# Kernel optimization log

Hardware: AMD Instinct MI355X
Metric: run time of the kernel (lower is better)

Reference implementation:

```python
import jax, jax.numpy as jnp
import numpy as np

# Izhikevich params (regular spiking), Euler step with dt=1
A, B_P, C, D, V_TH, DT = 0.02, 0.2, -65.0, 8.0, 30.0, 1.0


def _izh_scan(currents):
    """Run an Izhikevich cell over time. currents: [T, B, F] -> spikes [T, B, F]."""
    shp = currents.shape[1:]
    v0 = jnp.full(shp, C, dtype=currents.dtype)
    u0 = jnp.full(shp, B_P * C, dtype=currents.dtype)

    def step(state, i_t):
        v, u = state
        v = v + DT * (0.04 * v * v + 5.0 * v + 140.0 - u + i_t)
        u = u + DT * A * (B_P * v - u)
        z = (v >= V_TH).astype(currents.dtype)  # spike (heaviside)
        v = jnp.where(z > 0, C, v)               # reset
        u = u + z * D
        return (v, u), z

    (vT, uT), spikes = jax.lax.scan(step, (v0, u0), currents)
    return spikes, (vT, uT)


def setup_inputs() -> dict:
    key = jax.random.key(0)
    k1, k2, k3, k4, k5 = jax.random.split(key, 5)
    T, B, F_IN, F_HID = 2048, 8192, 4, 2
    xs = jax.random.normal(k1, (T, B, F_IN), dtype=jnp.float32)
    # PyTorch Linear default init: U(-1/sqrt(fan_in), 1/sqrt(fan_in)); scaled normal is fine for a baseline
    W_in = jax.random.normal(k2, (F_HID, F_IN), dtype=jnp.float32) * 0.5
    b_in = jax.random.normal(k3, (F_HID,), dtype=jnp.float32) * 0.5
    W_out = jax.random.normal(k4, (1, F_HID), dtype=jnp.float32) * 0.5
    b_out = jax.random.normal(k5, (1,), dtype=jnp.float32) * 0.5
    return {"xs": xs, "W_in": W_in, "b_in": b_in, "W_out": W_out, "b_out": b_out}


def reference(xs, W_in, b_in, W_out, b_out):
    # input linear: [T,B,4] @ [4,2] -> [T,B,2]
    h = jnp.einsum('tbi,oi->tbo', xs, W_in) + b_in
    input_spikes, _ = _izh_scan(h)
    # output linear: [T,B,2] -> [T,B,1]
    y = jnp.einsum('tbi,oi->tbo', input_spikes, W_out) + b_out
    output_spikes, _ = _izh_scan(y)
    return output_spikes
```

## Files before the change

kernel.cpp:

```cpp
#include <hip/hip_runtime.h>

namespace {

constexpr int T   = 2048;
constexpr int B   = 8192;
constexpr int C   = 32;
constexpr int NCH = T / C;
constexpr int RD  = 16;

__device__ __forceinline__ void barrier_nodrain() {
    asm volatile("s_waitcnt lgkmcnt(0)\n\ts_barrier" ::: "memory");
}

struct IzhState {
    float vnp;
    float up;
    bool  spp;
};

__device__ __forceinline__ bool izh_step(IzhState& s, float I) {
#pragma clang fp contract(off)
    const float K0 = ((0.04f * (-65.0f)) * (-65.0f) + (5.0f * (-65.0f))) + 140.0f;
    float m2a = 0.04f * s.vnp;
    float m2  = m2a * s.vnp;
    float f5  = 5.0f * s.vnp;
    float s2A = (m2 + f5) + 140.0f;
    float s3A = s2A - s.up;
    float s4A = s3A + I;
    float vnA = s.vnp + s4A;
    float s3S = K0 - s.up;
    float s4S = s3S + I;
    float vnS = (-65.0f) + s4S;
    float vn  = s.spp ? vnS : vnA;
    bool  sp  = (vn >= 30.0f);
    float m4  = 0.2f * vn;
    float s5  = m4 - s.up;
    float tt  = 0.02f * s5;
    float un  = s.up + tt;
    float d8  = sp ? 8.0f : 0.0f;
    s.up  = un + d8;
    s.vnp = vn;
    s.spp = sp;
    return sp;
}

__global__ __launch_bounds__(192, 1) void izh3b(
    const float* __restrict__ xs,
    const float* __restrict__ W_in, const float* __restrict__ b_in,
    const float* __restrict__ W_out, const float* __restrict__ b_out,
    float* __restrict__ out)
{
    __shared__ float zbuf[2][2][C][64];
    const int lane = threadIdx.x & 63;
    const int wid  = threadIdx.x >> 6;
    const int b    = blockIdx.x * 64 + lane;

    if (wid < 2) {
#pragma clang fp contract(off)
        const float wa = W_in[wid * 4 + 0], wb = W_in[wid * 4 + 1];
        const float wc = W_in[wid * 4 + 2], wd = W_in[wid * 4 + 3];
        const float bi = b_in[wid];
        const float4* xp = reinterpret_cast<const float4*>(xs) + b;

        float4 ring[RD];
#pragma unroll
        for (int i = 0; i < RD; ++i) ring[i] = xp[(size_t)i * B];

        IzhState st{-65.0f, -13.0f, true};
        for (int r = 0; r < NCH; ++r) {
            const int p = r & 1;
#pragma unroll
            for (int j = 0; j < C; ++j) {
                const int t = r * C + j;
                const float4 x = ring[j & (RD - 1)];
                ring[j & (RD - 1)] = xp[(size_t)((t + RD) & (T - 1)) * B];
                float h = (((x.x * wa) + (x.y * wb)) + (x.z * wc)) + (x.w * wd);
                h = h + bi;
                bool sp = izh_step(st, h);
                zbuf[wid][p][j][lane] = sp ? 1.0f : 0.0f;
            }
            barrier_nodrain();
        }
    } else {
#pragma clang fp contract(off)
        const float wo0 = W_out[0], wo1 = W_out[1], bo = b_out[0];
        const float c00 = ((0.0f * wo0) + (0.0f * wo1)) + bo;
        const float c10 = ((1.0f * wo0) + (0.0f * wo1)) + bo;
        const float c01 = ((0.0f * wo0) + (1.0f * wo1)) + bo;
        const float c11 = ((1.0f * wo0) + (1.0f * wo1)) + bo;
        float* op = out + b;
        IzhState st{-65.0f, -13.0f, true};

        auto consume = [&](int kk) {
#pragma clang fp contract(off)
            const int p = kk & 1;
            float z0[C], z1[C];
#pragma unroll
            for (int j = 0; j < C; ++j) {
                z0[j] = zbuf[0][p][j][lane];
                z1[j] = zbuf[1][p][j][lane];
            }
#pragma unroll
            for (int j = 0; j < C; ++j) {
                float yt = (z1[j] != 0.0f) ? c11 : c10;
                float yf = (z1[j] != 0.0f) ? c01 : c00;
                float y  = (z0[j] != 0.0f) ? yt : yf;
                bool spo = izh_step(st, y);
                op[(size_t)(kk * C + j) * B] = spo ? 1.0f : 0.0f;
            }
        };

        for (int r = 0; r < NCH; ++r) {
            if (r > 0) consume(r - 1);
            barrier_nodrain();
        }
        consume(NCH - 1);
    }
}

}

extern "C" void kernel_launch(void* const* d_in, const int* in_sizes, int n_in,
                              void* d_out, int out_size, void* d_ws, size_t ws_size,
                              hipStream_t stream) {
    const float* xs    = (const float*)d_in[0];
    const float* W_in  = (const float*)d_in[1];
    const float* b_in  = (const float*)d_in[2];
    const float* W_out = (const float*)d_in[3];
    const float* b_out = (const float*)d_in[4];
    float* out = (float*)d_out;

    dim3 grid(B / 64), block(192);
    hipLaunchKernelGGL(izh3b, grid, block, 0, stream,
                       xs, W_in, b_in, W_out, b_out, out);
}
```

Baseline: 428.0 us.

## Merge two hidden-neuron waves into one wave using packed float2 math

The two producer wavefronts that each simulated one hidden Izhikevich neuron become a single wavefront that steps both neurons together with two-wide vector float math, which can map to packed FP32 instructions. The block shrinks from three waves to two, and the shared spike buffer is stored as interleaved float2. The xs prefetch ring depth is doubled. The aim is to cut per-step instruction count and halve the redundant global loads of xs, at the cost of more registers and a serial dependency chain per wave that may leave the producer as the bottleneck.

```diff
diff --git a/kernel.cpp b/kernel.cpp
--- a/kernel.cpp
+++ b/kernel.cpp
@@ -6,10 +6,51 @@
 constexpr int B   = 8192;
 constexpr int C   = 32;
 constexpr int NCH = T / C;
-constexpr int RD  = 16;
+constexpr int RD  = 32;
+
+typedef float v2f __attribute__((ext_vector_type(2)));
 
 __device__ __forceinline__ void barrier_nodrain() {
     asm volatile("s_waitcnt lgkmcnt(0)\n\ts_barrier" ::: "memory");
+}
+
+struct IzhState2 {
+    v2f  vnp;
+    v2f  up;
+    bool sx;
+    bool sy;
+};
+
+__device__ __forceinline__ v2f izh_step2(IzhState2& s, v2f I) {
+#pragma clang fp contract(off)
+    const float K0 = ((0.04f * (-65.0f)) * (-65.0f) + (5.0f * (-65.0f))) + 140.0f;
+    v2f m2a = 0.04f * s.vnp;
+    v2f m2  = m2a * s.vnp;
+    v2f f5  = 5.0f * s.vnp;
+    v2f s2A = (m2 + f5) + 140.0f;
+    v2f s3A = s2A - s.up;
+    v2f s4A = s3A + I;
+    v2f vnA = s.vnp + s4A;
+    v2f s3S = K0 - s.up;
+    v2f s4S = s3S + I;
+    v2f vnS = (-65.0f) + s4S;
+    v2f vn;
+    vn.x = s.sx ? vnS.x : vnA.x;
+    vn.y = s.sy ? vnS.y : vnA.y;
+    bool nx = vn.x >= 30.0f;
+    bool ny = vn.y >= 30.0f;
+    v2f m4 = 0.2f * vn;
+    v2f s5 = m4 - s.up;
+    v2f tt = 0.02f * s5;
+    v2f un = s.up + tt;
+    v2f d8;
+    d8.x = nx ? 8.0f : 0.0f;
+    d8.y = ny ? 8.0f : 0.0f;
+    s.up  = un + d8;
+    s.vnp = vn;
+    s.sx  = nx;
+    s.sy  = ny;
+    return d8 * 0.125f;
 }
 
 struct IzhState {
@@ -44,29 +85,35 @@
     return sp;
 }
 
-__global__ __launch_bounds__(192, 1) void izh3b(
+__global__ __launch_bounds__(128, 1) void izh2w(
     const float* __restrict__ xs,
     const float* __restrict__ W_in, const float* __restrict__ b_in,
     const float* __restrict__ W_out, const float* __restrict__ b_out,
     float* __restrict__ out)
 {
-    __shared__ float zbuf[2][2][C][64];
+    __shared__ v2f zbuf[2][C][64];
     const int lane = threadIdx.x & 63;
     const int wid  = threadIdx.x >> 6;
     const int b    = blockIdx.x * 64 + lane;
 
-    if (wid < 2) {
+    if (wid == 0) {
 #pragma clang fp contract(off)
-        const float wa = W_in[wid * 4 + 0], wb = W_in[wid * 4 + 1];
-        const float wc = W_in[wid * 4 + 2], wd = W_in[wid * 4 + 3];
-        const float bi = b_in[wid];
+        const v2f wa = { W_in[0], W_in[4] };
+        const v2f wb = { W_in[1], W_in[5] };
+        const v2f wc = { W_in[2], W_in[6] };
+        const v2f wd = { W_in[3], W_in[7] };
+        const v2f bi = { b_in[0], b_in[1] };
         const float4* xp = reinterpret_cast<const float4*>(xs) + b;
 
         float4 ring[RD];
 #pragma unroll
         for (int i = 0; i < RD; ++i) ring[i] = xp[(size_t)i * B];
 
-        IzhState st{-65.0f, -13.0f, true};
+        IzhState2 st;
+        st.vnp = (v2f){-65.0f, -65.0f};
+        st.up  = (v2f){-13.0f, -13.0f};
+        st.sx = true; st.sy = true;
+
         for (int r = 0; r < NCH; ++r) {
             const int p = r & 1;
 #pragma unroll
@@ -74,10 +121,9 @@
                 const int t = r * C + j;
                 const float4 x = ring[j & (RD - 1)];
                 ring[j & (RD - 1)] = xp[(size_t)((t + RD) & (T - 1)) * B];
-                float h = (((x.x * wa) + (x.y * wb)) + (x.z * wc)) + (x.w * wd);
+                v2f h = (((x.x * wa) + (x.y * wb)) + (x.z * wc)) + (x.w * wd);
                 h = h + bi;
-                bool sp = izh_step(st, h);
-                zbuf[wid][p][j][lane] = sp ? 1.0f : 0.0f;
+                zbuf[p][j][lane] = izh_step2(st, h);
             }
             barrier_nodrain();
         }
@@ -94,17 +140,14 @@
         auto consume = [&](int kk) {
 #pragma clang fp contract(off)
             const int p = kk & 1;
-            float z0[C], z1[C];
+            v2f z[C];
+#pragma unroll
+            for (int j = 0; j < C; ++j) z[j] = zbuf[p][j][lane];
 #pragma unroll
             for (int j = 0; j < C; ++j) {
-                z0[j] = zbuf[0][p][j][lane];
-                z1[j] = zbuf[1][p][j][lane];
-            }
-#pragma unroll
-            for (int j = 0; j < C; ++j) {
-                float yt = (z1[j] != 0.0f) ? c11 : c10;
-                float yf = (z1[j] != 0.0f) ? c01 : c00;
-                float y  = (z0[j] != 0.0f) ? yt : yf;
+                float yt = (z[j].y != 0.0f) ? c11 : c10;
+                float yf = (z[j].y != 0.0f) ? c01 : c00;
+                float y  = (z[j].x != 0.0f) ? yt : yf;
                 bool spo = izh_step(st, y);
                 op[(size_t)(kk * C + j) * B] = spo ? 1.0f : 0.0f;
             }
@@ -130,7 +173,7 @@
     const float* b_out = (const float*)d_in[4];
     float* out = (float*)d_out;
 
-    dim3 grid(B / 64), block(192);
-    hipLaunchKernelGGL(izh3b, grid, block, 0, stream,
+    dim3 grid(B / 64), block(128);
+    hipLaunchKernelGGL(izh2w, grid, block, 0, stream,
                        xs, W_in, b_in, W_out, b_out, out);
 }
```

Result: slower. 510.1 us (+19.2%).

## Split Izhikevich pipeline into six specialized waves with LDS chunk handoff

Applied to the files above, without the earlier changes.

Restructures the per-block work from three waves into six: two loader waves compute the input linear layer, two waves run the hidden Izhikevich recurrences, one wave computes the output linear layer and stores results, and one wave runs the output neuron recurrence. Stages pass 32-step chunks through double-buffered float4 LDS buffers, so global loads, the linear maps and global stores are taken off the serial recurrence critical path. The neuron step is also reformulated with selects instead of computing both branches. This adds more barriers, LDS traffic and pipeline fill latency, and doubles the register ring depth in the loader waves.

```diff
diff --git a/kernel.cpp b/kernel.cpp
--- a/kernel.cpp
+++ b/kernel.cpp
@@ -6,7 +6,7 @@
 constexpr int B   = 8192;
 constexpr int C   = 32;
 constexpr int NCH = T / C;
-constexpr int RD  = 16;
+constexpr int RD  = 32;
 
 __device__ __forceinline__ void barrier_nodrain() {
     asm volatile("s_waitcnt lgkmcnt(0)\n\ts_barrier" ::: "memory");
@@ -18,20 +18,18 @@
     bool  spp;
 };
 
-__device__ __forceinline__ bool izh_step(IzhState& s, float I) {
+__device__ __forceinline__ float izh_step(IzhState& s, float I) {
 #pragma clang fp contract(off)
     const float K0 = ((0.04f * (-65.0f)) * (-65.0f) + (5.0f * (-65.0f))) + 140.0f;
     float m2a = 0.04f * s.vnp;
     float m2  = m2a * s.vnp;
     float f5  = 5.0f * s.vnp;
     float s2A = (m2 + f5) + 140.0f;
-    float s3A = s2A - s.up;
-    float s4A = s3A + I;
-    float vnA = s.vnp + s4A;
-    float s3S = K0 - s.up;
-    float s4S = s3S + I;
-    float vnS = (-65.0f) + s4S;
-    float vn  = s.spp ? vnS : vnA;
+    float pre = s.spp ? K0 : s2A;
+    float bse = s.spp ? -65.0f : s.vnp;
+    float s3  = pre - s.up;
+    float s4  = s3 + I;
+    float vn  = bse + s4;
     bool  sp  = (vn >= 30.0f);
     float m4  = 0.2f * vn;
     float s5  = m4 - s.up;
@@ -41,80 +39,148 @@
     s.up  = un + d8;
     s.vnp = vn;
     s.spp = sp;
-    return sp;
-}
-
-__global__ __launch_bounds__(192, 1) void izh3b(
+    return d8;
+}
+
+__global__ __launch_bounds__(384, 1) void izh6w(
     const float* __restrict__ xs,
     const float* __restrict__ W_in, const float* __restrict__ b_in,
     const float* __restrict__ W_out, const float* __restrict__ b_out,
     float* __restrict__ out)
 {
-    __shared__ float zbuf[2][2][C][64];
+    __shared__ float4 hbuf[2][2][8][64];
+    __shared__ float4 dbuf[2][2][8][64];
+    __shared__ float4 ybuf[2][8][64];
+    __shared__ float4 obuf[2][8][64];
     const int lane = threadIdx.x & 63;
     const int wid  = threadIdx.x >> 6;
     const int b    = blockIdx.x * 64 + lane;
 
-    if (wid < 2) {
-#pragma clang fp contract(off)
-        const float wa = W_in[wid * 4 + 0], wb = W_in[wid * 4 + 1];
-        const float wc = W_in[wid * 4 + 2], wd = W_in[wid * 4 + 3];
-        const float bi = b_in[wid];
+    if (wid >= 4) {
+#pragma clang fp contract(off)
+        const int n = wid - 4;
+        const float wa = W_in[n * 4 + 0], wb = W_in[n * 4 + 1];
+        const float wc = W_in[n * 4 + 2], wd = W_in[n * 4 + 3];
+        const float bi = b_in[n];
         const float4* xp = reinterpret_cast<const float4*>(xs) + b;
 
         float4 ring[RD];
 #pragma unroll
         for (int i = 0; i < RD; ++i) ring[i] = xp[(size_t)i * B];
 
+        {
+            float4 hr[8];
+#pragma unroll
+            for (int j = 0; j < C; ++j) {
+                const float4 x = ring[j];
+                ring[j] = xp[(size_t)((j + RD) & (T - 1)) * B];
+                float h = ((((x.x * wa) + (x.y * wb)) + (x.z * wc)) + (x.w * wd)) + bi;
+                reinterpret_cast<float*>(&hr[j >> 2])[j & 3] = h;
+            }
+#pragma unroll
+            for (int q = 0; q < 8; ++q) hbuf[n][0][q][lane] = hr[q];
+        }
+        barrier_nodrain();
+
+        for (int rr = 0; rr < NCH + 3; ++rr) {
+            if (rr + 1 < NCH) {
+                const int c = rr + 1, p = c & 1;
+                float4 hr[8];
+#pragma unroll
+                for (int j = 0; j < C; ++j) {
+                    const int t = c * C + j;
+                    const float4 x = ring[j];
+                    ring[j] = xp[(size_t)((t + RD) & (T - 1)) * B];
+                    float h = ((((x.x * wa) + (x.y * wb)) + (x.z * wc)) + (x.w * wd)) + bi;
+                    reinterpret_cast<float*>(&hr[j >> 2])[j & 3] = h;
+                }
+#pragma unroll
+                for (int q = 0; q < 8; ++q) hbuf[n][p][q][lane] = hr[q];
+            }
+            barrier_nodrain();
+        }
+    } else if (wid < 2) {
+#pragma clang fp contract(off)
+        const int n = wid;
         IzhState st{-65.0f, -13.0f, true};
-        for (int r = 0; r < NCH; ++r) {
-            const int p = r & 1;
-#pragma unroll
-            for (int j = 0; j < C; ++j) {
-                const int t = r * C + j;
-                const float4 x = ring[j & (RD - 1)];
-                ring[j & (RD - 1)] = xp[(size_t)((t + RD) & (T - 1)) * B];
-                float h = (((x.x * wa) + (x.y * wb)) + (x.z * wc)) + (x.w * wd);
-                h = h + bi;
-                bool sp = izh_step(st, h);
-                zbuf[wid][p][j][lane] = sp ? 1.0f : 0.0f;
+        barrier_nodrain();
+        for (int rr = 0; rr < NCH + 3; ++rr) {
+            if (rr < NCH) {
+                const int p = rr & 1;
+                float4 hr[8];
+#pragma unroll
+                for (int q = 0; q < 8; ++q) hr[q] = hbuf[n][p][q][lane];
+                float4 dr[8];
+#pragma unroll
+                for (int j = 0; j < C; ++j) {
+                    float h  = reinterpret_cast<const float*>(&hr[j >> 2])[j & 3];
+                    float d8 = izh_step(st, h);
+                    reinterpret_cast<float*>(&dr[j >> 2])[j & 3] = d8;
+                }
+#pragma unroll
+                for (int q = 0; q < 8; ++q) dbuf[n][p][q][lane] = dr[q];
+            }
+            barrier_nodrain();
+        }
+    } else if (wid == 2) {
+#pragma clang fp contract(off)
+        IzhState st{-65.0f, -13.0f, true};
+        barrier_nodrain();
+        for (int rr = 0; rr < NCH + 3; ++rr) {
+            if (rr >= 2 && rr <= NCH + 1) {
+                const int c = rr - 2, p = c & 1;
+                float4 yr[8];
+#pragma unroll
+                for (int q = 0; q < 8; ++q) yr[q] = ybuf[p][q][lane];
+                float4 orr[8];
+#pragma unroll
+                for (int j = 0; j < C; ++j) {
+                    float y  = reinterpret_cast<const float*>(&yr[j >> 2])[j & 3];
+                    float d8 = izh_step(st, y);
+                    reinterpret_cast<float*>(&orr[j >> 2])[j & 3] = d8 * 0.125f;
+                }
+#pragma unroll
+                for (int q = 0; q < 8; ++q) obuf[p][q][lane] = orr[q];
             }
             barrier_nodrain();
         }
     } else {
 #pragma clang fp contract(off)
         const float wo0 = W_out[0], wo1 = W_out[1], bo = b_out[0];
-        const float c00 = ((0.0f * wo0) + (0.0f * wo1)) + bo;
-        const float c10 = ((1.0f * wo0) + (0.0f * wo1)) + bo;
-        const float c01 = ((0.0f * wo0) + (1.0f * wo1)) + bo;
-        const float c11 = ((1.0f * wo0) + (1.0f * wo1)) + bo;
         float* op = out + b;
-        IzhState st{-65.0f, -13.0f, true};
-
-        auto consume = [&](int kk) {
-#pragma clang fp contract(off)
-            const int p = kk & 1;
-            float z0[C], z1[C];
-#pragma unroll
-            for (int j = 0; j < C; ++j) {
-                z0[j] = zbuf[0][p][j][lane];
-                z1[j] = zbuf[1][p][j][lane];
-            }
-#pragma unroll
-            for (int j = 0; j < C; ++j) {
-                float yt = (z1[j] != 0.0f) ? c11 : c10;
-                float yf = (z1[j] != 0.0f) ? c01 : c00;
-                float y  = (z0[j] != 0.0f) ? yt : yf;
-                bool spo = izh_step(st, y);
-                op[(size_t)(kk * C + j) * B] = spo ? 1.0f : 0.0f;
-            }
-        };
-
-        for (int r = 0; r < NCH; ++r) {
-            if (r > 0) consume(r - 1);
-            barrier_nodrain();
-        }
-        consume(NCH - 1);
+        barrier_nodrain();
+        for (int rr = 0; rr < NCH + 3; ++rr) {
+            if (rr >= 1 && rr <= NCH) {
+                const int c = rr - 1, p = c & 1;
+                float4 a0r[8], a1r[8];
+#pragma unroll
+                for (int q = 0; q < 8; ++q) a0r[q] = dbuf[0][p][q][lane];
+#pragma unroll
+                for (int q = 0; q < 8; ++q) a1r[q] = dbuf[1][p][q][lane];
+                float4 yr[8];
+#pragma unroll
+                for (int j = 0; j < C; ++j) {
+                    float z0 = reinterpret_cast<const float*>(&a0r[j >> 2])[j & 3] * 0.125f;
+                    float z1 = reinterpret_cast<const float*>(&a1r[j >> 2])[j & 3] * 0.125f;
+                    float y  = ((z0 * wo0) + (z1 * wo1)) + bo;
+                    reinterpret_cast<float*>(&yr[j >> 2])[j & 3] = y;
+                }
+#pragma unroll
+                for (int q = 0; q < 8; ++q) ybuf[p][q][lane] = yr[q];
+            }
+            if (rr >= 3) {
+                const int c = rr - 3, p = c & 1;
+                float4 orr[8];
+#pragma unroll
+                for (int q = 0; q < 8; ++q) orr[q] = obuf[p][q][lane];
+#pragma unroll
+                for (int j = 0; j < C; ++j) {
+                    op[(size_t)(c * C + j) * B] =
+                        reinterpret_cast<const float*>(&orr[j >> 2])[j & 3];
+                }
+            }
+            barrier_nodrain();
+        }
     }
 }
 
@@ -130,7 +196,7 @@
     const float* b_out = (const float*)d_in[4];
     float* out = (float*)d_out;
 
-    dim3 grid(B / 64), block(192);
-    hipLaunchKernelGGL(izh3b, grid, block, 0, stream,
+    dim3 grid(B / 64), block(384);
+    hipLaunchKernelGGL(izh6w, grid, block, 0, stream,
                        xs, W_in, b_in, W_out, b_out, out);
 }
```

New measurement: 480.3 us. 1.12x slower.
